# Kernel tuning notes

Measured on AMD Instinct MI355X. Metric: run time of the kernel, lower is better.

The kernel has to match this reference:

```python
import jax, jax.numpy as jnp
from jax import lax
import numpy as np


def _double_swish(x):
    # DoubleSwish(x) = x * sigmoid(x - 1)
    return x * jax.nn.sigmoid(x - 1.0)


def setup_inputs() -> dict:
    key = jax.random.key(0)
    ks = jax.random.split(key, 32)
    L, N, E, H, DFF, K = 1024, 4, 512, 8, 2048, 31
    d = E // (2 * H)  # head_dim = embed_dim // (num_heads * 2) = 32

    def g(i, shape, scale):
        return jax.random.normal(ks[i], shape, dtype=jnp.float32) * scale

    return {
        "src": g(0, (L, N, E), 1.0),
        "pos_emb": g(1, (1, 2 * L - 1, E), 1.0),
        "attn_scores_in": g(2, (N, L, L, H), 0.1),
        # attention params
        "w_in": g(3, (3 * E // 2, E), E ** -0.5),
        "b_in": g(4, (3 * E // 2,), 0.01),
        "w_pos": g(5, (E // 2, E), E ** -0.5),
        "pos_bias_u": g(6, (H, d), 0.05),
        "pos_bias_v": g(7, (H, d), 0.05),
        "proj_in": jnp.eye(H, dtype=jnp.float32) + g(8, (H, H), 0.1),
        "proj_out": g(9, (H, H), 0.1),
        "w_out": g(10, (E, E // 2), 0.05 * (E // 2) ** -0.5),  # ScaledLinear initial_scale=0.05
        "b_out": g(11, (E,), 0.01),
        # macaron FFN
        "w_ff1m": g(12, (DFF, E), E ** -0.5),
        "b_ff1m": g(13, (DFF,), 0.01),
        "w_ff2m": g(14, (E, DFF), 0.25 * DFF ** -0.5),
        "b_ff2m": g(15, (E,), 0.01),
        # final FFN
        "w_ff1": g(16, (DFF, E), E ** -0.5),
        "b_ff1": g(17, (DFF,), 0.01),
        "w_ff2": g(18, (E, DFF), 0.25 * DFF ** -0.5),
        "b_ff2": g(19, (E,), 0.01),
        # conv module
        "w_pw1": g(20, (2 * E, E), E ** -0.5),
        "b_pw1": g(21, (2 * E,), 0.01),
        "w_dw": g(22, (E, K), K ** -0.5),
        "b_dw": g(23, (E,), 0.01),
        "w_pw2": g(24, (E, E), 0.05 * E ** -0.5),  # ScaledConv1d initial_scale=0.05
        "b_pw2": g(25, (E,), 0.01),
        "norm_eps": jnp.array(0.25, dtype=jnp.float32),  # BasicNorm learned log-eps
    }


def reference(src, pos_emb, attn_scores_in, w_in, b_in, w_pos, pos_bias_u, pos_bias_v,
              proj_in, proj_out, w_out, b_out, w_ff1m, b_ff1m, w_ff2m, b_ff2m,
              w_ff1, b_ff1, w_ff2, b_ff2, w_pw1, b_pw1, w_dw, b_dw, w_pw2, b_pw2, norm_eps):
    L, N, E = src.shape
    H, d = pos_bias_u.shape
    K = w_dw.shape[1]

    def ff(x, w1, b1, w2, b2):
        return _double_swish(x @ w1.T + b1) @ w2.T + b2

    # macaron feed-forward (ActivationBalancer + dropout are identity at eval)
    x = src + ff(src, w_ff1m, b_ff1m, w_ff2m, b_ff2m)

    # --- rel-pos multi-head self-attention ---
    qkv = x @ w_in.T + b_in                          # (L,N,3E/2)
    q, k, v = jnp.split(qkv, 3, axis=-1)             # each (L,N,E/2)
    q = q.reshape(L, N, H, d).transpose(1, 2, 0, 3)  # (N,H,L,d)
    k = k.reshape(L, N, H, d).transpose(1, 2, 0, 3)
    v = v.reshape(L, N, H, d).transpose(1, 2, 0, 3)
    p = (pos_emb @ w_pos.T).reshape(2 * L - 1, H, d)  # (2L-1,H,d)

    ac = jnp.einsum('nhld,nhsd->nhls', q + pos_bias_u[None, :, None, :], k)
    bd = jnp.einsum('nhld,mhd->nhlm', q + pos_bias_v[None, :, None, :], p)  # (N,H,L,2L-1)
    # rel_shift: out[b,h,i,j] = bd[b,h,i,(L-1)-i+j]
    idx = (L - 1) - jnp.arange(L)[:, None] + jnp.arange(L)[None, :]  # (L,L)
    bd = jnp.take_along_axis(bd, idx[None, None], axis=-1)            # (N,H,L,L)

    scaling = d ** -0.5
    scores_in = jnp.einsum('nlsh,hg->ngls', attn_scores_in, proj_in)  # project then (N,H,L,L)
    total = (ac + bd) * scaling + scores_in
    attn = jax.nn.softmax(total, axis=-1)
    ctx = jnp.einsum('nhls,nhsd->nhld', attn, v)
    ctx = ctx.transpose(2, 0, 1, 3).reshape(L, N, E // 2)
    attn_out = ctx @ w_out.T + b_out
    scores_out = jnp.einsum('nhls,hg->nlsg', total, proj_out) + attn_scores_in
    x = x + attn_out

    # --- convolution module ---
    xc = x.transpose(1, 2, 0)                                        # (N,C,L)
    h = jnp.einsum('ncl,oc->nol', xc, w_pw1) + b_pw1[None, :, None]  # pointwise 1x1 -> 2C
    a, b = jnp.split(h, 2, axis=1)
    h = a * jax.nn.sigmoid(b)                                        # GLU(dim=1)
    pad = (K - 1) // 2
    h = lax.conv_general_dilated(h, w_dw[:, None, :], (1,), [(pad, pad)],
                                 feature_group_count=E,
                                 dimension_numbers=('NCH', 'OIH', 'NCH')) + b_dw[None, :, None]
    h = _double_swish(h)
    h = jnp.einsum('ncl,oc->nol', h, w_pw2) + b_pw2[None, :, None]
    x = x + h.transpose(2, 0, 1)

    # final feed-forward + BasicNorm
    x = x + ff(x, w_ff1, b_ff1, w_ff2, b_ff2)
    x = x * lax.rsqrt(jnp.mean(x * x, axis=-1, keepdims=True) + jnp.exp(norm_eps))
    return (x, scores_out)
```

## Files before the change

kernel.cpp:

```cpp
#include <hip/hip_runtime.h>

#define DEV_INLINE __device__ __forceinline__

typedef short bf16x8 __attribute__((ext_vector_type(8)));
typedef float f32x4 __attribute__((ext_vector_type(4)));
typedef unsigned short u16x8 __attribute__((ext_vector_type(8)));
typedef _Float16 f16x8 __attribute__((ext_vector_type(8)));
typedef _Float16 f16x2 __attribute__((ext_vector_type(2)));

DEV_INLINE float sigmoidf_(float x) { return 1.f / (1.f + __expf(-x)); }
DEV_INLINE unsigned short f2bf(float x) {
    unsigned int u = __float_as_uint(x);
    unsigned int r = (u + 0x7FFFu + ((u >> 16) & 1u)) >> 16;
    return (unsigned short)r;
}
DEV_INLINE float bf2f(unsigned short u) {
    return __uint_as_float(((unsigned int)u) << 16);
}
DEV_INLINE float fdot2_(f16x2 a, f16x2 b, float c) {
#if __has_builtin(__builtin_amdgcn_fdot2)
    return __builtin_amdgcn_fdot2(a, b, c, false);
#else
    return c + (float)a[0] * (float)b[0] + (float)a[1] * (float)b[1];
#endif
}
#define SL(v, k) __builtin_shufflevector(v, v, 2 * (k), 2 * (k) + 1)

struct CastJobs {
    const float4* src[11];
    ushort4* dst[11];
    int end[11];
};

__global__ __launch_bounds__(256) void cast_all_kernel(CastJobs jobs, int total4)
{
    int gi = blockIdx.x * 256 + threadIdx.x;
    if (gi >= total4) return;
    int s = 0, base = 0;
    while (gi >= jobs.end[s]) { base = jobs.end[s]; s++; }
    int li = gi - base;
    float4 v = jobs.src[s][li];
    ushort4 o = {f2bf(v.x), f2bf(v.y), f2bf(v.z), f2bf(v.w)};
    jobs.dst[s][li] = o;
}

template<int ACT, int RES, int WF32, int WBF>
__global__ __launch_bounds__(256) void mfma_gemm(
    const unsigned short* __restrict__ A, const unsigned short* __restrict__ B,
    const float* __restrict__ bias, const float* __restrict__ res,
    float* __restrict__ C, unsigned short* __restrict__ Cb, int M, int N, int K)
{
    __shared__ __align__(16) unsigned short As[128 * 32];
    __shared__ __align__(16) unsigned short Bs[128 * 32];

    const int t = threadIdx.x;
    const int lane = t & 63, wave = t >> 6;
    const int wr = wave >> 1, wc = wave & 1;
    const int lr = lane & 15, lk = lane >> 4;
    const int m0 = blockIdx.y * 128, n0 = blockIdx.x * 128;

    f32x4 acc[4][4] = {};

    for (int k0 = 0; k0 < K; k0 += 32) {
#pragma unroll
        for (int c = 0; c < 2; c++) {
            int bo = t * 16 + c * 4096;
            int row = bo >> 6;
            int col = (bo & 63) >> 1;
            __builtin_amdgcn_global_load_lds(
                (const __attribute__((address_space(1))) void*)(A + (size_t)(m0 + row) * K + k0 + col),
                (__attribute__((address_space(3))) void*)(As + (bo >> 1)), 16, 0, 0);
            __builtin_amdgcn_global_load_lds(
                (const __attribute__((address_space(1))) void*)(B + (size_t)(n0 + row) * K + k0 + col),
                (__attribute__((address_space(3))) void*)(Bs + (bo >> 1)), 16, 0, 0);
        }
        __syncthreads();

        bf16x8 af[4], bfr[4];
#pragma unroll
        for (int mi = 0; mi < 4; mi++)
            af[mi] = *(const bf16x8*)(As + (wr * 64 + mi * 16 + lr) * 32 + lk * 8);
#pragma unroll
        for (int nj = 0; nj < 4; nj++)
            bfr[nj] = *(const bf16x8*)(Bs + (wc * 64 + nj * 16 + lr) * 32 + lk * 8);
#pragma unroll
        for (int mi = 0; mi < 4; mi++)
#pragma unroll
            for (int nj = 0; nj < 4; nj++)
                acc[mi][nj] = __builtin_amdgcn_mfma_f32_16x16x32_bf16(
                    af[mi], bfr[nj], acc[mi][nj], 0, 0, 0);
        __syncthreads();
    }

#pragma unroll
    for (int nj = 0; nj < 4; nj++) {
        int col = n0 + wc * 64 + nj * 16 + lr;
        float bv = bias ? bias[col] : 0.f;
#pragma unroll
        for (int mi = 0; mi < 4; mi++) {
            int row = m0 + wr * 64 + mi * 16 + lk * 4;
#pragma unroll
            for (int j = 0; j < 4; j++) {
                int r = row + j;
                if (r >= M) continue;
                float v = acc[mi][nj][j] + bv;
                if (ACT) v = v * sigmoidf_(v - 1.f);
                size_t off = (size_t)r * N + col;
                if (RES) v += res[off];
                if (WF32) C[off] = v;
                if (WBF) Cb[off] = f2bf(v);
            }
        }
    }
}

template<int ACT, int RES, int WF32, int WBF>
__global__ __launch_bounds__(256) void mfma_gemm_n64(
    const unsigned short* __restrict__ A, const unsigned short* __restrict__ B,
    const float* __restrict__ bias, const float* __restrict__ res,
    float* __restrict__ C, unsigned short* __restrict__ Cb, int M, int N, int K)
{
    __shared__ __align__(16) unsigned short As[128 * 32];
    __shared__ __align__(16) unsigned short Bs[64 * 32];

    const int t = threadIdx.x;
    const int lane = t & 63, wave = t >> 6;
    const int wr = wave >> 1, wc = wave & 1;
    const int lr = lane & 15, lk = lane >> 4;
    const int m0 = blockIdx.y * 128, n0 = blockIdx.x * 64;

    f32x4 acc[4][2] = {};

    for (int k0 = 0; k0 < K; k0 += 32) {
#pragma unroll
        for (int c = 0; c < 2; c++) {
            int bo = t * 16 + c * 4096;
            int row = bo >> 6;
            int col = (bo & 63) >> 1;
            __builtin_amdgcn_global_load_lds(
                (const __attribute__((address_space(1))) void*)(A + (size_t)(m0 + row) * K + k0 + col),
                (__attribute__((address_space(3))) void*)(As + (bo >> 1)), 16, 0, 0);
        }
        {
            int bo = t * 16;
            int row = bo >> 6;
            int col = (bo & 63) >> 1;
            __builtin_amdgcn_global_load_lds(
                (const __attribute__((address_space(1))) void*)(B + (size_t)(n0 + row) * K + k0 + col),
                (__attribute__((address_space(3))) void*)(Bs + (bo >> 1)), 16, 0, 0);
        }
        __syncthreads();

        bf16x8 af[4], bfr[2];
#pragma unroll
        for (int mi = 0; mi < 4; mi++)
            af[mi] = *(const bf16x8*)(As + (wr * 64 + mi * 16 + lr) * 32 + lk * 8);
#pragma unroll
        for (int nj = 0; nj < 2; nj++)
            bfr[nj] = *(const bf16x8*)(Bs + (wc * 32 + nj * 16 + lr) * 32 + lk * 8);
#pragma unroll
        for (int mi = 0; mi < 4; mi++)
#pragma unroll
            for (int nj = 0; nj < 2; nj++)
                acc[mi][nj] = __builtin_amdgcn_mfma_f32_16x16x32_bf16(
                    af[mi], bfr[nj], acc[mi][nj], 0, 0, 0);
        __syncthreads();
    }

#pragma unroll
    for (int nj = 0; nj < 2; nj++) {
        int col = n0 + wc * 32 + nj * 16 + lr;
        float bv = bias ? bias[col] : 0.f;
#pragma unroll
        for (int mi = 0; mi < 4; mi++) {
            int row = m0 + wr * 64 + mi * 16 + lk * 4;
#pragma unroll
            for (int j = 0; j < 4; j++) {
                int r = row + j;
                float v = acc[mi][nj][j] + bv;
                if (ACT) v = v * sigmoidf_(v - 1.f);
                size_t off = (size_t)r * N + col;
                if (RES) v += res[off];
                if (WF32) C[off] = v;
                if (WBF) Cb[off] = f2bf(v);
            }
        }
    }
}

__global__ __launch_bounds__(256) void split_kernel(
    const float* __restrict__ qkv,
    const float* __restrict__ pbu, const float* __restrict__ pbv,
    _Float16* __restrict__ quh, _Float16* __restrict__ qvh,
    _Float16* __restrict__ kh, unsigned short* __restrict__ vt)
{
    int idx = blockIdx.x * 256 + threadIdx.x;
    int dd = idx & 31;
    int l  = (idx >> 5) & 1023;
    int nh = idx >> 15;
    int h  = nh & 7;
    int n  = nh >> 3;
    size_t base = ((size_t)l * 4 + n) * 768 + h * 32 + dd;
    float q = qkv[base];
    quh[idx] = (_Float16)(q + pbu[h * 32 + dd]);
    qvh[idx] = (_Float16)(q + pbv[h * 32 + dd]);
    kh[idx]  = (_Float16)qkv[base + 256];
    vt[(size_t)nh * 32768 + dd * 1024 + l] = f2bf(qkv[base + 512]);
}

__global__ __launch_bounds__(256) void repack_p_kernel(
    const float* __restrict__ pb, _Float16* __restrict__ p2h)
{
    int idx = blockIdx.x * 256 + threadIdx.x;
    if (idx >= 2047 * 256) return;
    int dd = idx & 31;
    int h  = (idx >> 5) & 7;
    int m  = idx >> 8;
    p2h[((size_t)h * 2047 + m) * 32 + dd] = (_Float16)pb[idx];
}

__global__ __launch_bounds__(256) void scores_kernel(
    const _Float16* __restrict__ quh, const _Float16* __restrict__ qvh,
    const _Float16* __restrict__ kh, const _Float16* __restrict__ p2h,
    unsigned short* __restrict__ totb)
{
    __shared__ __align__(16) float4 Qu4h[64 * 5];
    __shared__ __align__(16) float4 Qv4h[64 * 5];
    __shared__ __align__(16) float4 K4h[64 * 5];
    __shared__ __align__(16) float4 P4h[127 * 5 + 3];
    __shared__ __align__(16) unsigned short staged[64][72];

    const int t = threadIdx.x;
    const int tx = t & 15, ty = t >> 4;
    const int j0 = blockIdx.x * 64, i0 = blockIdx.y * 64;
    const int nh = blockIdx.z;
    const int n = nh >> 3, h = nh & 7;
    const int m_base = 960 - i0 + j0;

    const float4* qug = (const float4*)(quh + ((size_t)nh * 1024 + i0) * 32);
    const float4* qvg = (const float4*)(qvh + ((size_t)nh * 1024 + i0) * 32);
    const float4* kg  = (const float4*)(kh + ((size_t)nh * 1024 + j0) * 32);
    const float4* pg  = (const float4*)(p2h + ((size_t)h * 2047 + m_base) * 32);

    {
        int r = t >> 2, c = t & 3;
        Qu4h[r * 5 + c] = qug[t];
        Qv4h[r * 5 + c] = qvg[t];
        K4h[r * 5 + c]  = kg[t];
    }
#pragma unroll
    for (int cc = 0; cc < 2; cc++) {
        int fi = t + 256 * cc;
        if (fi < 508) {
            int r = fi >> 2, c = fi & 3;
            P4h[r * 5 + c] = pg[fi];
        }
    }
    __syncthreads();

    float acc[4][4] = {};
    const int pbase = 63 + tx - ty;

#pragma unroll
    for (int dg = 0; dg < 4; dg++) {
        f16x8 qu_[4], qv_[4], k_[4], p_[7];
#pragma unroll
        for (int ii = 0; ii < 4; ii++) {
            qu_[ii] = __builtin_bit_cast(f16x8, Qu4h[(ty + 16 * ii) * 5 + dg]);
            qv_[ii] = __builtin_bit_cast(f16x8, Qv4h[(ty + 16 * ii) * 5 + dg]);
        }
#pragma unroll
        for (int jj = 0; jj < 4; jj++)
            k_[jj] = __builtin_bit_cast(f16x8, K4h[(tx + 16 * jj) * 5 + dg]);
#pragma unroll
        for (int s = 0; s < 7; s++)
            p_[s] = __builtin_bit_cast(f16x8, P4h[(pbase + 16 * (s - 3)) * 5 + dg]);
#pragma unroll
        for (int ii = 0; ii < 4; ii++)
#pragma unroll
            for (int jj = 0; jj < 4; jj++) {
                f16x8 a = qu_[ii], b = k_[jj];
                f16x8 av = qv_[ii], pv = p_[jj - ii + 3];
                float r = acc[ii][jj];
                r = fdot2_(SL(a, 0), SL(b, 0), r);
                r = fdot2_(SL(a, 1), SL(b, 1), r);
                r = fdot2_(SL(a, 2), SL(b, 2), r);
                r = fdot2_(SL(a, 3), SL(b, 3), r);
                r = fdot2_(SL(av, 0), SL(pv, 0), r);
                r = fdot2_(SL(av, 1), SL(pv, 1), r);
                r = fdot2_(SL(av, 2), SL(pv, 2), r);
                r = fdot2_(SL(av, 3), SL(pv, 3), r);
                acc[ii][jj] = r;
            }
    }

    const float scale = 0.17677669529663687f;
#pragma unroll
    for (int ii = 0; ii < 4; ii++)
#pragma unroll
        for (int jj = 0; jj < 4; jj++)
            staged[ty + 16 * ii][tx + 16 * jj] = f2bf(acc[ii][jj] * scale);
    __syncthreads();

    int r = t >> 2, q = t & 3;
    unsigned short* o = totb + (((size_t)(n * 1024 + i0 + r)) * 8 + h) * 1024 + j0;
    u16x8 v0 = *(const u16x8*)&staged[r][q * 16];
    u16x8 v1 = *(const u16x8*)&staged[r][q * 16 + 8];
    *(u16x8*)(o + q * 16) = v0;
    *(u16x8*)(o + q * 16 + 8) = v1;
}

__global__ __launch_bounds__(256) void attn_finish_kernel(
    unsigned short* __restrict__ totb, const float* __restrict__ as_,
    const float* __restrict__ proj_in, const float* __restrict__ proj_out,
    float* __restrict__ out_s)
{
    __shared__ float pin_s[64], po_s[64];
    __shared__ float redbuf[4][8];

    const int t = threadIdx.x;
    const int n = blockIdx.x >> 10;
    const int i = blockIdx.x & 1023;
    const int j0 = t * 4;
    const int wave = t >> 6, lane = t & 63;

    if (t < 64) { pin_s[t] = proj_in[t]; po_s[t] = proj_out[t]; }

    unsigned short* tbase = totb + ((size_t)(n * 1024 + i)) * 8192;
    const float4* as4 = (const float4*)(as_ + (((size_t)n * 1024 + i) * 1024 + j0) * 8);
    float4* os4 = (float4*)(out_s + (((size_t)n * 1024 + i) * 1024 + j0) * 8);

    ushort4 tu[8];
#pragma unroll
    for (int h = 0; h < 8; h++)
        tu[h] = *(const ushort4*)(tbase + h * 1024 + j0);
    float4 av4[8];
#pragma unroll
    for (int c = 0; c < 8; c++) av4[c] = as4[c];
    __syncthreads();

    float th[8][4];
#pragma unroll
    for (int h = 0; h < 8; h++) {
        th[h][0] = bf2f(tu[h].x); th[h][1] = bf2f(tu[h].y);
        th[h][2] = bf2f(tu[h].z); th[h][3] = bf2f(tu[h].w);
    }

#pragma unroll
    for (int jj = 0; jj < 4; jj++) {
        float4 alo = av4[jj * 2], ahi = av4[jj * 2 + 1];
        float ag[8] = {alo.x, alo.y, alo.z, alo.w, ahi.x, ahi.y, ahi.z, ahi.w};
#pragma unroll
        for (int h = 0; h < 8; h++) {
            float si = 0.f;
#pragma unroll
            for (int g = 0; g < 8; g++) si += ag[g] * pin_s[g * 8 + h];
            th[h][jj] += si;
        }
        float so[8];
#pragma unroll
        for (int g = 0; g < 8; g++) {
            float s = ag[g];
#pragma unroll
            for (int h = 0; h < 8; h++) s += th[h][jj] * po_s[h * 8 + g];
            so[g] = s;
        }
        float4 o0 = {so[0], so[1], so[2], so[3]};
        float4 o1 = {so[4], so[5], so[6], so[7]};
        os4[jj * 2] = o0;
        os4[jj * 2 + 1] = o1;
    }

    float sm[8];
#pragma unroll
    for (int h = 0; h < 8; h++) {
        float s = 0.f;
#pragma unroll
        for (int jj = 0; jj < 4; jj++) {
            th[h][jj] = __expf(th[h][jj]);
            s += th[h][jj];
        }
        sm[h] = s;
    }
#pragma unroll
    for (int d = 1; d < 64; d <<= 1)
#pragma unroll
        for (int h = 0; h < 8; h++) sm[h] += __shfl_xor(sm[h], d);
    if (lane == 0)
#pragma unroll
        for (int h = 0; h < 8; h++) redbuf[wave][h] = sm[h];
    __syncthreads();

#pragma unroll
    for (int h = 0; h < 8; h++) {
        float rs = 1.f / (redbuf[0][h] + redbuf[1][h] + redbuf[2][h] + redbuf[3][h]);
        ushort4 o = {f2bf(th[h][0] * rs), f2bf(th[h][1] * rs),
                     f2bf(th[h][2] * rs), f2bf(th[h][3] * rs)};
        *(ushort4*)(tbase + h * 1024 + j0) = o;
    }
}

__global__ __launch_bounds__(256) void ctx_mfma_kernel(
    const unsigned short* __restrict__ attnb, const unsigned short* __restrict__ vt,
    unsigned short* __restrict__ ctx_b)
{
    __shared__ __align__(16) unsigned short As[128 * 32];
    __shared__ __align__(16) unsigned short Bs[32 * 32];

    const int t = threadIdx.x;
    const int lane = t & 63, wave = t >> 6;
    const int lr = lane & 15, lk = lane >> 4;
    const int i0 = blockIdx.x * 128;
    const int nh = blockIdx.y;
    const int n = nh >> 3, h = nh & 7;

    const unsigned short* Bbase = vt + (size_t)nh * 32768;

    f32x4 acc[2][2] = {};

    for (int k0 = 0; k0 < 1024; k0 += 32) {
#pragma unroll
        for (int c = 0; c < 2; c++) {
            int bo = t * 16 + c * 4096;
            int row = bo >> 6;
            int col = (bo & 63) >> 1;
            __builtin_amdgcn_global_load_lds(
                (const __attribute__((address_space(1))) void*)(
                    attnb + (((size_t)(n * 1024 + i0 + row)) * 8 + h) * 1024 + k0 + col),
                (__attribute__((address_space(3))) void*)(As + (bo >> 1)), 16, 0, 0);
        }
        if (t < 128) {
            int bo = t * 16;
            int row = bo >> 6;
            int col = (bo & 63) >> 1;
            __builtin_amdgcn_global_load_lds(
                (const __attribute__((address_space(1))) void*)(Bbase + (size_t)row * 1024 + k0 + col),
                (__attribute__((address_space(3))) void*)(Bs + (bo >> 1)), 16, 0, 0);
        }
        __syncthreads();

        bf16x8 af[2], bf_[2];
#pragma unroll
        for (int mi = 0; mi < 2; mi++)
            af[mi] = *(const bf16x8*)(As + (wave * 32 + mi * 16 + lr) * 32 + lk * 8);
#pragma unroll
        for (int nj = 0; nj < 2; nj++)
            bf_[nj] = *(const bf16x8*)(Bs + (nj * 16 + lr) * 32 + lk * 8);
#pragma unroll
        for (int mi = 0; mi < 2; mi++)
#pragma unroll
            for (int nj = 0; nj < 2; nj++)
                acc[mi][nj] = __builtin_amdgcn_mfma_f32_16x16x32_bf16(
                    af[mi], bf_[nj], acc[mi][nj], 0, 0, 0);
        __syncthreads();
    }

#pragma unroll
    for (int nj = 0; nj < 2; nj++) {
        int d = nj * 16 + lr;
#pragma unroll
        for (int mi = 0; mi < 2; mi++) {
            int ibase = i0 + wave * 32 + mi * 16 + lk * 4;
#pragma unroll
            for (int j = 0; j < 4; j++) {
                int i = ibase + j;
                ctx_b[((size_t)i * 4 + n) * 256 + h * 32 + d] = f2bf(acc[mi][nj][j]);
            }
        }
    }
}

__global__ __launch_bounds__(256) void glu_kernel(
    const unsigned short* __restrict__ h1, unsigned short* __restrict__ g)
{
    int idx4 = blockIdx.x * 256 + threadIdx.x;
    int r = idx4 >> 7, c4 = idx4 & 127;
    const ushort4* row = (const ushort4*)(h1 + (size_t)r * 1024);
    ushort4 a = row[c4];
    ushort4 b = row[128 + c4];
    ushort4 o = {f2bf(bf2f(a.x) * sigmoidf_(bf2f(b.x))),
                 f2bf(bf2f(a.y) * sigmoidf_(bf2f(b.y))),
                 f2bf(bf2f(a.z) * sigmoidf_(bf2f(b.z))),
                 f2bf(bf2f(a.w) * sigmoidf_(bf2f(b.w)))};
    ((ushort4*)g)[idx4] = o;
}

__global__ __launch_bounds__(256) void dwconv_kernel(
    const unsigned short* __restrict__ g, const float* __restrict__ w_dw,
    const float* __restrict__ b_dw, unsigned short* __restrict__ out)
{
    int idx = blockIdx.x * 256 + threadIdx.x;
    int c = idx & 511;
    int r = idx >> 9;
    int nn = r & 3, l = r >> 2;
    float acc = b_dw[c];
#pragma unroll
    for (int kk = 0; kk < 31; kk++) {
        int l2 = l + kk - 15;
        if (l2 >= 0 && l2 < 1024)
            acc += bf2f(g[(((size_t)l2 * 4 + nn) << 9) + c]) * w_dw[c * 31 + kk];
    }
    out[idx] = f2bf(acc * sigmoidf_(acc - 1.f));
}

__global__ __launch_bounds__(256) void norm_kernel(
    const float* __restrict__ x, const float* __restrict__ eps_p,
    float* __restrict__ out)
{
    int r = blockIdx.x, t = threadIdx.x;
    float a = x[(size_t)r * 512 + t];
    float b = x[(size_t)r * 512 + 256 + t];
    float ss = a * a + b * b;
#pragma unroll
    for (int d = 1; d < 64; d <<= 1) ss += __shfl_xor(ss, d);
    __shared__ float red[4];
    if ((t & 63) == 0) red[t >> 6] = ss;
    __syncthreads();
    float tot = red[0] + red[1] + red[2] + red[3];
    float scale = rsqrtf(tot * (1.f / 512.f) + __expf(eps_p[0]));
    out[(size_t)r * 512 + t] = a * scale;
    out[(size_t)r * 512 + 256 + t] = b * scale;
}

extern "C" void kernel_launch(void* const* d_in, const int* in_sizes, int n_in,
                              void* d_out, int out_size, void* d_ws, size_t ws_size,
                              hipStream_t stream)
{
    const float* src   = (const float*)d_in[0];
    const float* pos   = (const float*)d_in[1];
    const float* as_   = (const float*)d_in[2];
    const float* w_in  = (const float*)d_in[3];
    const float* b_in  = (const float*)d_in[4];
    const float* w_pos = (const float*)d_in[5];
    const float* pbu   = (const float*)d_in[6];
    const float* pbv   = (const float*)d_in[7];
    const float* prin  = (const float*)d_in[8];
    const float* prout = (const float*)d_in[9];
    const float* w_out = (const float*)d_in[10];
    const float* b_out = (const float*)d_in[11];
    const float* w_ff1m = (const float*)d_in[12];
    const float* b_ff1m = (const float*)d_in[13];
    const float* w_ff2m = (const float*)d_in[14];
    const float* b_ff2m = (const float*)d_in[15];
    const float* w_ff1 = (const float*)d_in[16];
    const float* b_ff1 = (const float*)d_in[17];
    const float* w_ff2 = (const float*)d_in[18];
    const float* b_ff2 = (const float*)d_in[19];
    const float* w_pw1 = (const float*)d_in[20];
    const float* b_pw1 = (const float*)d_in[21];
    const float* w_dw  = (const float*)d_in[22];
    const float* b_dw  = (const float*)d_in[23];
    const float* w_pw2 = (const float*)d_in[24];
    const float* b_pw2 = (const float*)d_in[25];
    const float* neps  = (const float*)d_in[26];

    float* out_x = (float*)d_out;
    float* out_s = (float*)d_out + 2097152;

    float* ws = (float*)d_ws;
    float* xbuf = ws;
    float* U    = xbuf + 2097152;
    float* sbbf = U + 6291456;
    float* xb16f= sbbf + 1048576;
    float* qkvb = xb16f + 1048576;
    float* qu   = qkvb + 3145728;
    float* qv   = qu + 1048576;
    float* kbuf = qv + 1048576;
    float* vbuf = kbuf + 1048576;
    float* pbuf = vbuf + 1048576;
    float* posbf= pbuf + 524288;
    float* totf = posbf + 524288;
    float* Wreg = totf + 16777216;

    unsigned short* hb16  = (unsigned short*)U;
    unsigned short* gbuf  = (unsigned short*)(U + 4194304);
    unsigned short* sbb   = (unsigned short*)sbbf;
    unsigned short* dbufb = (unsigned short*)sbbf;
    unsigned short* xb16  = (unsigned short*)xb16f;
    unsigned short* ctxb  = (unsigned short*)qu;
    unsigned short* posb  = (unsigned short*)posbf;
    unsigned short* totb  = (unsigned short*)totf;
    unsigned short* vt    = (unsigned short*)vbuf;
    _Float16*       quh   = (_Float16*)qu;
    _Float16*       qvh   = (_Float16*)qv;
    _Float16*       kh    = (_Float16*)kbuf;
    _Float16*       p2h   = (_Float16*)qkvb;

    float* wp = Wreg;
    unsigned short* wff1m_b = (unsigned short*)wp; wp += 524288;
    unsigned short* wff2m_b = (unsigned short*)wp; wp += 524288;
    unsigned short* win_b   = (unsigned short*)wp; wp += 196608;
    unsigned short* wpos_b  = (unsigned short*)wp; wp += 65536;
    unsigned short* wout_b  = (unsigned short*)wp; wp += 65536;
    unsigned short* wpw1_b  = (unsigned short*)wp; wp += 262144;
    unsigned short* wpw2_b  = (unsigned short*)wp; wp += 131072;
    unsigned short* wff1_b  = (unsigned short*)wp; wp += 524288;
    unsigned short* wff2_b  = (unsigned short*)wp; wp += 524288;

    dim3 blk(256);
    const int M = 4096;

    {
        CastJobs jobs;
        const float* srcs[11] = {src, pos, w_ff1m, w_ff2m, w_in, w_pos,
                                 w_out, w_pw1, w_pw2, w_ff1, w_ff2};
        unsigned short* dsts[11] = {sbb, posb, wff1m_b, wff2m_b, win_b, wpos_b,
                                    wout_b, wpw1_b, wpw2_b, wff1_b, wff2_b};
        int n4s[11] = {524288, 262016, 262144, 262144, 98304, 32768,
                       32768, 131072, 65536, 262144, 262144};
        int cum = 0;
        for (int s = 0; s < 11; s++) {
            jobs.src[s] = (const float4*)srcs[s];
            jobs.dst[s] = (ushort4*)dsts[s];
            cum += n4s[s];
            jobs.end[s] = cum;
        }
        cast_all_kernel<<<(cum + 255) / 256, blk, 0, stream>>>(jobs, cum);
    }

    mfma_gemm<1,0,0,1><<<dim3(16, 32), blk, 0, stream>>>(
        sbb, wff1m_b, b_ff1m, nullptr, nullptr, hb16, M, 2048, 512);
    mfma_gemm_n64<0,1,1,1><<<dim3(8, 32), blk, 0, stream>>>(
        hb16, wff2m_b, b_ff2m, src, xbuf, xb16, M, 512, 2048);

    mfma_gemm_n64<0,0,1,0><<<dim3(12, 32), blk, 0, stream>>>(
        xb16, win_b, b_in, nullptr, qkvb, nullptr, M, 768, 512);
    split_kernel<<<4096, blk, 0, stream>>>(qkvb, pbu, pbv, quh, qvh, kh, vt);
    mfma_gemm<0,0,1,0><<<dim3(2, 16), blk, 0, stream>>>(
        posb, wpos_b, nullptr, nullptr, pbuf, nullptr, 2047, 256, 512);
    repack_p_kernel<<<2047, blk, 0, stream>>>(pbuf, p2h);
    scores_kernel<<<dim3(16, 16, 32), blk, 0, stream>>>(quh, qvh, kh, p2h, totb);
    attn_finish_kernel<<<4096, blk, 0, stream>>>(totb, as_, prin, prout, out_s);
    ctx_mfma_kernel<<<dim3(8, 32), blk, 0, stream>>>(totb, vt, ctxb);
    mfma_gemm_n64<0,1,1,1><<<dim3(8, 32), blk, 0, stream>>>(
        ctxb, wout_b, b_out, xbuf, xbuf, xb16, M, 512, 256);

    mfma_gemm<0,0,0,1><<<dim3(8, 32), blk, 0, stream>>>(
        xb16, wpw1_b, b_pw1, nullptr, nullptr, hb16, M, 1024, 512);
    glu_kernel<<<2048, blk, 0, stream>>>(hb16, gbuf);
    dwconv_kernel<<<8192, blk, 0, stream>>>(gbuf, w_dw, b_dw, dbufb);
    mfma_gemm_n64<0,1,1,1><<<dim3(8, 32), blk, 0, stream>>>(
        dbufb, wpw2_b, b_pw2, xbuf, xbuf, xb16, M, 512, 512);

    mfma_gemm<1,0,0,1><<<dim3(16, 32), blk, 0, stream>>>(
        xb16, wff1_b, b_ff1, nullptr, nullptr, hb16, M, 2048, 512);
    mfma_gemm_n64<0,1,1,0><<<dim3(8, 32), blk, 0, stream>>>(
        hb16, wff2_b, b_ff2, xbuf, xbuf, nullptr, M, 512, 2048);
    norm_kernel<<<4096, blk, 0, stream>>>(xbuf, neps, out_x);
}
```

Measured before the change: 499.7 us.

## Compute relative-position attention scores with bf16 MFMA instead of fp16 dot2

The scores kernel now computes both the content term (q+u)·k and the positional term (q+v)·p as bf16 MFMA tiles, replacing the per-thread fp16 fdot2 loops. The positional term is computed as a full 64x128 band product and then shifted diagonally through LDS to apply the relative-position offset. The q, k and p inputs are converted to bf16 and loaded with direct global-to-LDS loads. This trades fp16 precision for bf16, does about twice the positional FLOPs, and adds an extra LDS staging pass in exchange for matrix-core throughput.

```diff
diff --git a/kernel.cpp b/kernel.cpp
--- a/kernel.cpp
+++ b/kernel.cpp
@@ -1,12 +1,12 @@
 #include <hip/hip_runtime.h>
 
 #define DEV_INLINE __device__ __forceinline__
+#define AS1 __attribute__((address_space(1)))
+#define AS3 __attribute__((address_space(3)))
 
 typedef short bf16x8 __attribute__((ext_vector_type(8)));
 typedef float f32x4 __attribute__((ext_vector_type(4)));
 typedef unsigned short u16x8 __attribute__((ext_vector_type(8)));
-typedef _Float16 f16x8 __attribute__((ext_vector_type(8)));
-typedef _Float16 f16x2 __attribute__((ext_vector_type(2)));
 
 DEV_INLINE float sigmoidf_(float x) { return 1.f / (1.f + __expf(-x)); }
 DEV_INLINE unsigned short f2bf(float x) {
@@ -17,14 +17,6 @@
 DEV_INLINE float bf2f(unsigned short u) {
     return __uint_as_float(((unsigned int)u) << 16);
 }
-DEV_INLINE float fdot2_(f16x2 a, f16x2 b, float c) {
-#if __has_builtin(__builtin_amdgcn_fdot2)
-    return __builtin_amdgcn_fdot2(a, b, c, false);
-#else
-    return c + (float)a[0] * (float)b[0] + (float)a[1] * (float)b[1];
-#endif
-}
-#define SL(v, k) __builtin_shufflevector(v, v, 2 * (k), 2 * (k) + 1)
 
 struct CastJobs {
     const float4* src[11];
@@ -68,11 +60,11 @@
             int row = bo >> 6;
             int col = (bo & 63) >> 1;
             __builtin_amdgcn_global_load_lds(
-                (const __attribute__((address_space(1))) void*)(A + (size_t)(m0 + row) * K + k0 + col),
-                (__attribute__((address_space(3))) void*)(As + (bo >> 1)), 16, 0, 0);
+                (const AS1 void*)(A + (size_t)(m0 + row) * K + k0 + col),
+                (AS3 void*)(As + (bo >> 1)), 16, 0, 0);
             __builtin_amdgcn_global_load_lds(
-                (const __attribute__((address_space(1))) void*)(B + (size_t)(n0 + row) * K + k0 + col),
-                (__attribute__((address_space(3))) void*)(Bs + (bo >> 1)), 16, 0, 0);
+                (const AS1 void*)(B + (size_t)(n0 + row) * K + k0 + col),
+                (AS3 void*)(Bs + (bo >> 1)), 16, 0, 0);
         }
         __syncthreads();
 
@@ -138,16 +130,16 @@
             int row = bo >> 6;
             int col = (bo & 63) >> 1;
             __builtin_amdgcn_global_load_lds(
-                (const __attribute__((address_space(1))) void*)(A + (size_t)(m0 + row) * K + k0 + col),
-                (__attribute__((address_space(3))) void*)(As + (bo >> 1)), 16, 0, 0);
+                (const AS1 void*)(A + (size_t)(m0 + row) * K + k0 + col),
+                (AS3 void*)(As + (bo >> 1)), 16, 0, 0);
         }
         {
             int bo = t * 16;
             int row = bo >> 6;
             int col = (bo & 63) >> 1;
             __builtin_amdgcn_global_load_lds(
-                (const __attribute__((address_space(1))) void*)(B + (size_t)(n0 + row) * K + k0 + col),
-                (__attribute__((address_space(3))) void*)(Bs + (bo >> 1)), 16, 0, 0);
+                (const AS1 void*)(B + (size_t)(n0 + row) * K + k0 + col),
+                (AS3 void*)(Bs + (bo >> 1)), 16, 0, 0);
         }
         __syncthreads();
 
@@ -191,8 +183,8 @@
 __global__ __launch_bounds__(256) void split_kernel(
     const float* __restrict__ qkv,
     const float* __restrict__ pbu, const float* __restrict__ pbv,
-    _Float16* __restrict__ quh, _Float16* __restrict__ qvh,
-    _Float16* __restrict__ kh, unsigned short* __restrict__ vt)
+    unsigned short* __restrict__ qub, unsigned short* __restrict__ qvb,
+    unsigned short* __restrict__ kb, unsigned short* __restrict__ vt)
 {
     int idx = blockIdx.x * 256 + threadIdx.x;
     int dd = idx & 31;
@@ -202,112 +194,118 @@
     int n  = nh >> 3;
     size_t base = ((size_t)l * 4 + n) * 768 + h * 32 + dd;
     float q = qkv[base];
-    quh[idx] = (_Float16)(q + pbu[h * 32 + dd]);
-    qvh[idx] = (_Float16)(q + pbv[h * 32 + dd]);
-    kh[idx]  = (_Float16)qkv[base + 256];
+    qub[idx] = f2bf(q + pbu[h * 32 + dd]);
+    qvb[idx] = f2bf(q + pbv[h * 32 + dd]);
+    kb[idx]  = f2bf(qkv[base + 256]);
     vt[(size_t)nh * 32768 + dd * 1024 + l] = f2bf(qkv[base + 512]);
 }
 
 __global__ __launch_bounds__(256) void repack_p_kernel(
-    const float* __restrict__ pb, _Float16* __restrict__ p2h)
+    const float* __restrict__ pb, unsigned short* __restrict__ p2b)
 {
     int idx = blockIdx.x * 256 + threadIdx.x;
     if (idx >= 2047 * 256) return;
     int dd = idx & 31;
     int h  = (idx >> 5) & 7;
     int m  = idx >> 8;
-    p2h[((size_t)h * 2047 + m) * 32 + dd] = (_Float16)pb[idx];
+    p2b[((size_t)h * 2047 + m) * 32 + dd] = f2bf(pb[idx]);
 }
 
 __global__ __launch_bounds__(256) void scores_kernel(
-    const _Float16* __restrict__ quh, const _Float16* __restrict__ qvh,
-    const _Float16* __restrict__ kh, const _Float16* __restrict__ p2h,
+    const unsigned short* __restrict__ qub_, const unsigned short* __restrict__ qvb_,
+    const unsigned short* __restrict__ kb_, const unsigned short* __restrict__ p2b_,
     unsigned short* __restrict__ totb)
 {
-    __shared__ __align__(16) float4 Qu4h[64 * 5];
-    __shared__ __align__(16) float4 Qv4h[64 * 5];
-    __shared__ __align__(16) float4 K4h[64 * 5];
-    __shared__ __align__(16) float4 P4h[127 * 5 + 3];
-    __shared__ __align__(16) unsigned short staged[64][72];
+    __shared__ __align__(16) char smem[49920];
+    unsigned short* Qu = (unsigned short*)smem;
+    unsigned short* Qv = (unsigned short*)(smem + 4096);
+    unsigned short* Kt = (unsigned short*)(smem + 8192);
+    unsigned short* Pt = (unsigned short*)(smem + 12288);
+    float* AC = (float*)smem;
+    float* C2 = (float*)(smem + 16640);
 
     const int t = threadIdx.x;
-    const int tx = t & 15, ty = t >> 4;
+    const int lane = t & 63, wave = t >> 6;
+    const int wr = wave >> 1, wc = wave & 1;
+    const int lr = lane & 15, lk = lane >> 4;
     const int j0 = blockIdx.x * 64, i0 = blockIdx.y * 64;
     const int nh = blockIdx.z;
     const int n = nh >> 3, h = nh & 7;
     const int m_base = 960 - i0 + j0;
 
-    const float4* qug = (const float4*)(quh + ((size_t)nh * 1024 + i0) * 32);
-    const float4* qvg = (const float4*)(qvh + ((size_t)nh * 1024 + i0) * 32);
-    const float4* kg  = (const float4*)(kh + ((size_t)nh * 1024 + j0) * 32);
-    const float4* pg  = (const float4*)(p2h + ((size_t)h * 2047 + m_base) * 32);
-
-    {
-        int r = t >> 2, c = t & 3;
-        Qu4h[r * 5 + c] = qug[t];
-        Qv4h[r * 5 + c] = qvg[t];
-        K4h[r * 5 + c]  = kg[t];
-    }
-#pragma unroll
-    for (int cc = 0; cc < 2; cc++) {
-        int fi = t + 256 * cc;
-        if (fi < 508) {
-            int r = fi >> 2, c = fi & 3;
-            P4h[r * 5 + c] = pg[fi];
-        }
-    }
+    const unsigned short* qug = qub_ + ((size_t)nh * 1024 + i0) * 32;
+    const unsigned short* qvg = qvb_ + ((size_t)nh * 1024 + i0) * 32;
+    const unsigned short* kg  = kb_ + ((size_t)nh * 1024 + j0) * 32;
+    const unsigned short* pg  = p2b_ + ((size_t)h * 2047 + m_base) * 32;
+
+    __builtin_amdgcn_global_load_lds((const AS1 void*)(qug + t * 8),
+                                     (AS3 void*)(Qu + t * 8), 16, 0, 0);
+    __builtin_amdgcn_global_load_lds((const AS1 void*)(qvg + t * 8),
+                                     (AS3 void*)(Qv + t * 8), 16, 0, 0);
+    __builtin_amdgcn_global_load_lds((const AS1 void*)(kg + t * 8),
+                                     (AS3 void*)(Kt + t * 8), 16, 0, 0);
+#pragma unroll
+    for (int c = 0; c < 2; c++)
+        __builtin_amdgcn_global_load_lds((const AS1 void*)(pg + (t + 256 * c) * 8),
+                                         (AS3 void*)(Pt + (t + 256 * c) * 8), 16, 0, 0);
     __syncthreads();
 
-    float acc[4][4] = {};
-    const int pbase = 63 + tx - ty;
-
-#pragma unroll
-    for (int dg = 0; dg < 4; dg++) {
-        f16x8 qu_[4], qv_[4], k_[4], p_[7];
-#pragma unroll
-        for (int ii = 0; ii < 4; ii++) {
-            qu_[ii] = __builtin_bit_cast(f16x8, Qu4h[(ty + 16 * ii) * 5 + dg]);
-            qv_[ii] = __builtin_bit_cast(f16x8, Qv4h[(ty + 16 * ii) * 5 + dg]);
-        }
-#pragma unroll
-        for (int jj = 0; jj < 4; jj++)
-            k_[jj] = __builtin_bit_cast(f16x8, K4h[(tx + 16 * jj) * 5 + dg]);
-#pragma unroll
-        for (int s = 0; s < 7; s++)
-            p_[s] = __builtin_bit_cast(f16x8, P4h[(pbase + 16 * (s - 3)) * 5 + dg]);
-#pragma unroll
-        for (int ii = 0; ii < 4; ii++)
-#pragma unroll
-            for (int jj = 0; jj < 4; jj++) {
-                f16x8 a = qu_[ii], b = k_[jj];
-                f16x8 av = qv_[ii], pv = p_[jj - ii + 3];
-                float r = acc[ii][jj];
-                r = fdot2_(SL(a, 0), SL(b, 0), r);
-                r = fdot2_(SL(a, 1), SL(b, 1), r);
-                r = fdot2_(SL(a, 2), SL(b, 2), r);
-                r = fdot2_(SL(a, 3), SL(b, 3), r);
-                r = fdot2_(SL(av, 0), SL(pv, 0), r);
-                r = fdot2_(SL(av, 1), SL(pv, 1), r);
-                r = fdot2_(SL(av, 2), SL(pv, 2), r);
-                r = fdot2_(SL(av, 3), SL(pv, 3), r);
-                acc[ii][jj] = r;
-            }
-    }
+    bf16x8 aq[2], av[2], bk[2], bp[4];
+#pragma unroll
+    for (int f = 0; f < 2; f++) {
+        aq[f] = *(const bf16x8*)(Qu + (wr * 32 + f * 16 + lr) * 32 + lk * 8);
+        av[f] = *(const bf16x8*)(Qv + (wr * 32 + f * 16 + lr) * 32 + lk * 8);
+        bk[f] = *(const bf16x8*)(Kt + (wc * 32 + f * 16 + lr) * 32 + lk * 8);
+    }
+#pragma unroll
+    for (int f = 0; f < 4; f++)
+        bp[f] = *(const bf16x8*)(Pt + (wc * 64 + f * 16 + lr) * 32 + lk * 8);
+
+    f32x4 aacc[2][2] = {};
+    f32x4 bacc[2][4] = {};
+#pragma unroll
+    for (int fi = 0; fi < 2; fi++) {
+#pragma unroll
+        for (int fj = 0; fj < 2; fj++)
+            aacc[fi][fj] = __builtin_amdgcn_mfma_f32_16x16x32_bf16(
+                aq[fi], bk[fj], aacc[fi][fj], 0, 0, 0);
+#pragma unroll
+        for (int fj = 0; fj < 4; fj++)
+            bacc[fi][fj] = __builtin_amdgcn_mfma_f32_16x16x32_bf16(
+                av[fi], bp[fj], bacc[fi][fj], 0, 0, 0);
+    }
+    __syncthreads();
+
+#pragma unroll
+    for (int fi = 0; fi < 2; fi++)
+#pragma unroll
+        for (int fj = 0; fj < 2; fj++)
+#pragma unroll
+            for (int jj = 0; jj < 4; jj++)
+                AC[(wr * 32 + fi * 16 + lk * 4 + jj) * 65 + wc * 32 + fj * 16 + lr]
+                    = aacc[fi][fj][jj];
+#pragma unroll
+    for (int fi = 0; fi < 2; fi++)
+#pragma unroll
+        for (int fj = 0; fj < 4; fj++)
+#pragma unroll
+            for (int jj = 0; jj < 4; jj++)
+                C2[(wr * 32 + fi * 16 + lk * 4 + jj) * 130 + wc * 64 + fj * 16 + lr]
+                    = bacc[fi][fj][jj];
+    __syncthreads();
 
     const float scale = 0.17677669529663687f;
-#pragma unroll
-    for (int ii = 0; ii < 4; ii++)
-#pragma unroll
-        for (int jj = 0; jj < 4; jj++)
-            staged[ty + 16 * ii][tx + 16 * jj] = f2bf(acc[ii][jj] * scale);
-    __syncthreads();
-
     int r = t >> 2, q = t & 3;
-    unsigned short* o = totb + (((size_t)(n * 1024 + i0 + r)) * 8 + h) * 1024 + j0;
-    u16x8 v0 = *(const u16x8*)&staged[r][q * 16];
-    u16x8 v1 = *(const u16x8*)&staged[r][q * 16 + 8];
-    *(u16x8*)(o + q * 16) = v0;
-    *(u16x8*)(o + q * 16 + 8) = v1;
+    unsigned short ov[16];
+#pragma unroll
+    for (int c16 = 0; c16 < 16; c16++) {
+        int c = q * 16 + c16;
+        float v = AC[r * 65 + c] + C2[r * 130 + 63 + c - r];
+        ov[c16] = f2bf(v * scale);
+    }
+    unsigned short* o = totb + (((size_t)(n * 1024 + i0 + r)) * 8 + h) * 1024 + j0 + q * 16;
+    *(u16x8*)o = *(const u16x8*)&ov[0];
+    *(u16x8*)(o + 8) = *(const u16x8*)&ov[8];
 }
 
 __global__ __launch_bounds__(256) void attn_finish_kernel(
@@ -425,17 +423,17 @@
             int row = bo >> 6;
             int col = (bo & 63) >> 1;
             __builtin_amdgcn_global_load_lds(
-                (const __attribute__((address_space(1))) void*)(
+                (const AS1 void*)(
                     attnb + (((size_t)(n * 1024 + i0 + row)) * 8 + h) * 1024 + k0 + col),
-                (__attribute__((address_space(3))) void*)(As + (bo >> 1)), 16, 0, 0);
+                (AS3 void*)(As + (bo >> 1)), 16, 0, 0);
         }
         if (t < 128) {
             int bo = t * 16;
             int row = bo >> 6;
             int col = (bo & 63) >> 1;
             __builtin_amdgcn_global_load_lds(
-                (const __attribute__((address_space(1))) void*)(Bbase + (size_t)row * 1024 + k0 + col),
-                (__attribute__((address_space(3))) void*)(Bs + (bo >> 1)), 16, 0, 0);
+                (const AS1 void*)(Bbase + (size_t)row * 1024 + k0 + col),
+                (AS3 void*)(Bs + (bo >> 1)), 16, 0, 0);
         }
         __syncthreads();
 
@@ -581,10 +579,10 @@
     unsigned short* posb  = (unsigned short*)posbf;
     unsigned short* totb  = (unsigned short*)totf;
     unsigned short* vt    = (unsigned short*)vbuf;
-    _Float16*       quh   = (_Float16*)qu;
-    _Float16*       qvh   = (_Float16*)qv;
-    _Float16*       kh    = (_Float16*)kbuf;
-    _Float16*       p2h   = (_Float16*)qkvb;
+    unsigned short* qub   = (unsigned short*)qu;
+    unsigned short* qvb   = (unsigned short*)qv;
+    unsigned short* kb    = (unsigned short*)kbuf;
+    unsigned short* p2b   = (unsigned short*)qkvb;
 
     float* wp = Wreg;
     unsigned short* wff1m_b = (unsigned short*)wp; wp += 524288;
@@ -625,11 +623,11 @@
 
     mfma_gemm_n64<0,0,1,0><<<dim3(12, 32), blk, 0, stream>>>(
         xb16, win_b, b_in, nullptr, qkvb, nullptr, M, 768, 512);
-    split_kernel<<<4096, blk, 0, stream>>>(qkvb, pbu, pbv, quh, qvh, kh, vt);
+    split_kernel<<<4096, blk, 0, stream>>>(qkvb, pbu, pbv, qub, qvb, kb, vt);
     mfma_gemm<0,0,1,0><<<dim3(2, 16), blk, 0, stream>>>(
         posb, wpos_b, nullptr, nullptr, pbuf, nullptr, 2047, 256, 512);
-    repack_p_kernel<<<2047, blk, 0, stream>>>(pbuf, p2h);
-    scores_kernel<<<dim3(16, 16, 32), blk, 0, stream>>>(quh, qvh, kh, p2h, totb);
+    repack_p_kernel<<<2047, blk, 0, stream>>>(pbuf, p2b);
+    scores_kernel<<<dim3(16, 16, 32), blk, 0, stream>>>(qub, qvb, kb, p2b, totb);
     attn_finish_kernel<<<4096, blk, 0, stream>>>(totb, as_, prin, prout, out_s);
     ctx_mfma_kernel<<<dim3(8, 32), blk, 0, stream>>>(totb, vt, ctxb);
     mfma_gemm_n64<0,1,1,1><<<dim3(8, 32), blk, 0, stream>>>(
```

New measurement: 492.6 us. Within noise of the previous version (-1.4%).
